# Performance work log

Measured on AMD Instinct MI355X. Metric: run time of the kernel, lower is better.

## Reference

```python
import jax, jax.numpy as jnp
import numpy as np
from math import sqrt

D_MODEL = 1024
N_HEADS = 16
E = D_MODEL // N_HEADS  # d_keys = d_values = 64


def setup_inputs() -> dict:
    key = jax.random.key(0)
    ks = jax.random.split(key, 11)
    B, L, S = 2, 2048, 2048
    s = 1.0 / sqrt(D_MODEL)
    return {
        "queries": jax.random.normal(ks[0], (B, L, D_MODEL), jnp.float32),
        "keys": jax.random.normal(ks[1], (B, S, D_MODEL), jnp.float32),
        "values": jax.random.normal(ks[2], (B, S, D_MODEL), jnp.float32),
        "Wq": jax.random.normal(ks[3], (D_MODEL, D_MODEL), jnp.float32) * s,
        "bq": jnp.zeros((D_MODEL,), jnp.float32),
        "Wk": jax.random.normal(ks[4], (D_MODEL, D_MODEL), jnp.float32) * s,
        "bk": jnp.zeros((D_MODEL,), jnp.float32),
        "Wv": jax.random.normal(ks[5], (D_MODEL, D_MODEL), jnp.float32) * s,
        "bv": jnp.zeros((D_MODEL,), jnp.float32),
        "Wo": jax.random.normal(ks[6], (D_MODEL, D_MODEL), jnp.float32) * s,
        "bo": jnp.zeros((D_MODEL,), jnp.float32),
    }


def reference(queries, keys, values, Wq, bq, Wk, bk, Wv, bv, Wo, bo):
    B, L, _ = queries.shape
    S = keys.shape[1]
    H = N_HEADS
    # projections -> [B, L/S, H, E]
    q = (queries @ Wq + bq).reshape(B, L, H, E)
    k = (keys @ Wk + bk).reshape(B, S, H, E)
    v = (values @ Wv + bv).reshape(B, S, H, E)
    scale = 1.0 / sqrt(E)
    scores = jnp.einsum('blhe,bshe->bhls', q, k)  # [B,H,L,S]
    A = jax.nn.softmax(scale * scores, axis=-1)   # dropout = identity (eval)
    V = jnp.einsum('bhls,bshd->blhd', A, v)       # [B,L,H,E]
    out = V.reshape(B, L, H * E) @ Wo + bo
    return out
```

## Files before the change

kernel.cpp:

```cpp
#include <hip/hip_runtime.h>
#include <hip/hip_bf16.h>
#include <stdint.h>

#define BATCH 2
#define SEQ   2048
#define DM    1024
#define NH    16
#define EH    64
#define MROWS (BATCH*SEQ)

typedef __attribute__((ext_vector_type(8))) short  short8;
typedef __attribute__((ext_vector_type(4))) float  floatx4;
typedef __attribute__((ext_vector_type(8))) unsigned short ushort8v;
typedef __attribute__((ext_vector_type(4))) unsigned short ushort4v;

__device__ __forceinline__ unsigned short f2bf(float f) {
    return (unsigned short)((__float_as_uint(f) + 0x8000u) >> 16);
}

__device__ __forceinline__ void gload_lds16(const void* g, void* l) {
    __builtin_amdgcn_global_load_lds(
        (const __attribute__((address_space(1))) unsigned int*)g,
        (__attribute__((address_space(3))) unsigned int*)l, 16, 0, 0);
}

__global__ __launch_bounds__(256)
void transpose_w(const float* __restrict__ W0, const float* __restrict__ W1,
                 const float* __restrict__ W2, const float* __restrict__ W3,
                 unsigned short* __restrict__ T0, unsigned short* __restrict__ T1,
                 unsigned short* __restrict__ T2, unsigned short* __restrict__ T3,
                 int zbase)
{
    int z = zbase + blockIdx.z;
    const float* W = (z == 0) ? W0 : (z == 1) ? W1 : (z == 2) ? W2 : W3;
    unsigned short* T = (z == 0) ? T0 : (z == 1) ? T1 : (z == 2) ? T2 : T3;
    __shared__ float t[32][33];
    const int tid = threadIdx.x;
    const int k0 = blockIdx.y * 32, n0 = blockIdx.x * 32;
    {
        int r = tid >> 3, c4 = (tid & 7) * 4;
        float4 u = *(const float4*)&W[(size_t)(k0 + r) * DM + n0 + c4];
        t[r][c4 + 0] = u.x; t[r][c4 + 1] = u.y; t[r][c4 + 2] = u.z; t[r][c4 + 3] = u.w;
    }
    __syncthreads();
    {
        int n = tid >> 3, k4 = (tid & 7) * 4;
        ushort4v o;
        o[0] = f2bf(t[k4 + 0][n]); o[1] = f2bf(t[k4 + 1][n]);
        o[2] = f2bf(t[k4 + 2][n]); o[3] = f2bf(t[k4 + 3][n]);
        *(ushort4v*)&T[(size_t)(n0 + n) * DM + k0 + k4] = o;
    }
}

struct ProjArgs {
    const float* act[3];
    const unsigned short* wt[3];
    const float* bias[3];
    unsigned short* C[3];
    float oscale[3];
};

__global__ __launch_bounds__(256)
void proj_qkv(ProjArgs pa)
{
    const int z = blockIdx.z;
    const bool vt = (z == 2);
    const int linear = (int)(blockIdx.x + gridDim.x * blockIdx.y);
    int rb, cb;
    if (!vt) { rb = linear & 31; cb = linear >> 5; }
    else     { cb = linear & 31; rb = linear >> 5; }
    const int row0 = rb * 128, col0 = cb * 128;

    const float* act = pa.act[z];
    const unsigned short* wt = pa.wt[z];

    __shared__ unsigned short As[128 * 32];
    __shared__ unsigned short Bs[128 * 32];

    const int tid = threadIdx.x;
    const int lane = tid & 63, w = tid >> 6;
    const int lane15 = lane & 15, quad = lane >> 4;

    floatx4 acc[2][8] = {};

    for (int kt = 0; kt < DM; kt += 32) {
        __syncthreads();
        if (!vt) {
#pragma unroll
            for (int rr = 0; rr < 2; ++rr) {
                int c = rr * 256 + tid;
                int row = c >> 2, kel = (c & 3) * 8;
                const float* p = &act[(size_t)(row0 + row) * DM + kt + kel];
                float4 u0 = *(const float4*)p;
                float4 u1 = *(const float4*)(p + 4);
                ushort8v o8;
                o8[0] = f2bf(u0.x); o8[1] = f2bf(u0.y); o8[2] = f2bf(u0.z); o8[3] = f2bf(u0.w);
                o8[4] = f2bf(u1.x); o8[5] = f2bf(u1.y); o8[6] = f2bf(u1.z); o8[7] = f2bf(u1.w);
                *(ushort8v*)&As[(size_t)c * 8] = o8;
            }
#pragma unroll
            for (int rr = 0; rr < 2; ++rr) {
                int c = rr * 256 + w * 64 + lane;
                int row = c >> 2, kel = (c & 3) * 8;
                gload_lds16(&wt[(size_t)(col0 + row) * DM + kt + kel],
                            (char*)Bs + (size_t)(rr * 256 + w * 64) * 16);
            }
        } else {
#pragma unroll
            for (int rr = 0; rr < 2; ++rr) {
                int c = rr * 256 + w * 64 + lane;
                int row = c >> 2, kel = (c & 3) * 8;
                gload_lds16(&wt[(size_t)(row0 + row) * DM + kt + kel],
                            (char*)As + (size_t)(rr * 256 + w * 64) * 16);
            }
#pragma unroll
            for (int rr = 0; rr < 2; ++rr) {
                int c = rr * 256 + tid;
                int row = c >> 2, kel = (c & 3) * 8;
                const float* p = &act[(size_t)(col0 + row) * DM + kt + kel];
                float4 u0 = *(const float4*)p;
                float4 u1 = *(const float4*)(p + 4);
                ushort8v o8;
                o8[0] = f2bf(u0.x); o8[1] = f2bf(u0.y); o8[2] = f2bf(u0.z); o8[3] = f2bf(u0.w);
                o8[4] = f2bf(u1.x); o8[5] = f2bf(u1.y); o8[6] = f2bf(u1.z); o8[7] = f2bf(u1.w);
                *(ushort8v*)&Bs[(size_t)c * 8] = o8;
            }
        }
        __syncthreads();

        short8 af[2], bf[8];
#pragma unroll
        for (int i = 0; i < 2; ++i)
            af[i] = *(const short8*)&As[(w * 32 + i * 16 + lane15) * 32 + quad * 8];
#pragma unroll
        for (int j = 0; j < 8; ++j)
            bf[j] = *(const short8*)&Bs[(j * 16 + lane15) * 32 + quad * 8];
#pragma unroll
        for (int i = 0; i < 2; ++i)
#pragma unroll
            for (int j = 0; j < 8; ++j)
                acc[i][j] = __builtin_amdgcn_mfma_f32_16x16x32_bf16(af[i], bf[j], acc[i][j], 0, 0, 0);
    }

    const float* bias = pa.bias[z];
    const float os = pa.oscale[z];
    unsigned short* C = pa.C[z];
#pragma unroll
    for (int i = 0; i < 2; ++i) {
#pragma unroll
        for (int j = 0; j < 8; ++j) {
#pragma unroll
            for (int r = 0; r < 4; ++r) {
                int row = row0 + w * 32 + i * 16 + quad * 4 + r;
                int col = col0 + j * 16 + lane15;
                if (!vt) {
                    float v = (acc[i][j][r] + bias[col]) * os;
                    int b = row >> 11, l = row & (SEQ - 1);
                    int h = col >> 6,  e = col & (EH - 1);
                    C[((size_t)(b * NH + h) * SEQ + l) * EH + e] = f2bf(v);
                } else {
                    float v = acc[i][j][r] + bias[row];
                    int h = row >> 6,  e = row & (EH - 1);
                    int b = col >> 11, l = col & (SEQ - 1);
                    C[((size_t)(b * NH + h) * EH + e) * SEQ + l] = f2bf(v);
                }
            }
        }
    }
}

__global__ __launch_bounds__(256)
void gemm_out(const unsigned short* __restrict__ ctx,
              const unsigned short* __restrict__ WoT,
              const float* __restrict__ bo,
              float* __restrict__ out)
{
    const int linear = (int)(blockIdx.x + gridDim.x * blockIdx.y);
    const int rb = linear & 31, cb = linear >> 5;
    const int row0 = rb * 128, col0 = cb * 64;

    __shared__ unsigned short As[128 * 32];
    __shared__ unsigned short Bs[64 * 32];

    const int tid = threadIdx.x;
    const int lane = tid & 63, w = tid >> 6;
    const int lane15 = lane & 15, quad = lane >> 4;

    floatx4 acc[2][4] = {};

    for (int kt = 0; kt < DM; kt += 32) {
        __syncthreads();
#pragma unroll
        for (int rr = 0; rr < 2; ++rr) {
            int c = rr * 256 + w * 64 + lane;
            int row = c >> 2, kel = (c & 3) * 8;
            gload_lds16(&ctx[(size_t)(row0 + row) * DM + kt + kel],
                        (char*)As + (size_t)(rr * 256 + w * 64) * 16);
        }
        {
            int c = w * 64 + lane;
            int row = c >> 2, kel = (c & 3) * 8;
            gload_lds16(&WoT[(size_t)(col0 + row) * DM + kt + kel],
                        (char*)Bs + (size_t)(w * 64) * 16);
        }
        __syncthreads();

        short8 af[2], bf[4];
#pragma unroll
        for (int i = 0; i < 2; ++i)
            af[i] = *(const short8*)&As[(w * 32 + i * 16 + lane15) * 32 + quad * 8];
#pragma unroll
        for (int j = 0; j < 4; ++j)
            bf[j] = *(const short8*)&Bs[(j * 16 + lane15) * 32 + quad * 8];
#pragma unroll
        for (int i = 0; i < 2; ++i)
#pragma unroll
            for (int j = 0; j < 4; ++j)
                acc[i][j] = __builtin_amdgcn_mfma_f32_16x16x32_bf16(af[i], bf[j], acc[i][j], 0, 0, 0);
    }

#pragma unroll
    for (int i = 0; i < 2; ++i)
#pragma unroll
        for (int j = 0; j < 4; ++j)
#pragma unroll
            for (int r = 0; r < 4; ++r) {
                int row = row0 + w * 32 + i * 16 + quad * 4 + r;
                int col = col0 + j * 16 + lane15;
                out[(size_t)row * DM + col] = acc[i][j][r] + bo[col];
            }
}

__device__ __forceinline__ void stage_kv(const unsigned short* __restrict__ Kp,
                                         const unsigned short* __restrict__ Vp,
                                         int st, unsigned short* ksb, unsigned short* vsb,
                                         int w, int lane)
{
#pragma unroll
    for (int rr = 0; rr < 2; ++rr) {
        int p = rr * 256 + w * 64 + lane;
        int row = p >> 3;
        int gch = (p & 7) ^ (row & 7);
        gload_lds16(&Kp[(size_t)(st + row) * EH + gch * 8],
                    ksb + (size_t)(rr * 256 + w * 64) * 8);
        gload_lds16(&Vp[(size_t)row * SEQ + st + gch * 8],
                    vsb + (size_t)(rr * 256 + w * 64) * 8);
    }
}

__global__ __launch_bounds__(256)
void attn_mfma(const unsigned short* __restrict__ Qh,
               const unsigned short* __restrict__ Kh,
               const unsigned short* __restrict__ Vt,
               unsigned short* __restrict__ ctx)
{
    __shared__ unsigned short Ks[2][64 * 64];
    __shared__ unsigned short Vs[2][64 * 64];
    __shared__ unsigned short Ps[128][72];

    const int tid = threadIdx.x;
    const int lane = tid & 63, w = tid >> 6;
    const int lane15 = lane & 15, quad = lane >> 4;
    const int qt = blockIdx.x, h = blockIdx.y, b = blockIdx.z;
    const size_t bh = (size_t)(b * NH + h);
    const unsigned short* Kp = Kh + bh * SEQ * EH;
    const unsigned short* Vp = Vt + bh * EH * SEQ;

    short8 qf[2][2];
    {
        const unsigned short* Qp =
            Qh + (bh * SEQ + (size_t)qt * 128 + w * 32 + lane15) * EH;
#pragma unroll
        for (int ks = 0; ks < 2; ++ks) {
            qf[0][ks] = *(const short8*)(Qp + ks * 32 + quad * 8);
            qf[1][ks] = *(const short8*)(Qp + 16 * EH + ks * 32 + quad * 8);
        }
    }
    short8 ones;
#pragma unroll
    for (int i = 0; i < 8; ++i) ones[i] = (short)0x3F80;

    floatx4 o[2][4] = {};
    floatx4 lacc[2] = {};

    stage_kv(Kp, Vp, 0, Ks[0], Vs[0], w, lane);
    __syncthreads();
    int cur = 0;

    for (int st = 0; st < SEQ; st += 64) {
        int nxt = cur ^ 1;
        if (st + 64 < SEQ)
            stage_kv(Kp, Vp, st + 64, Ks[nxt], Vs[nxt], w, lane);
        const unsigned short* ksb = Ks[cur];
        const unsigned short* vsb = Vs[cur];

        floatx4 sacc[4][2] = {};
#pragma unroll
        for (int ts = 0; ts < 4; ++ts) {
#pragma unroll
            for (int ks = 0; ks < 2; ++ks) {
                short8 kf = *(const short8*)&ksb[((ts * 16 + lane15) << 6) +
                                                 ((((ks << 2) + quad) ^ (lane15 & 7)) << 3)];
                sacc[ts][0] = __builtin_amdgcn_mfma_f32_16x16x32_bf16(kf, qf[0][ks], sacc[ts][0], 0, 0, 0);
                sacc[ts][1] = __builtin_amdgcn_mfma_f32_16x16x32_bf16(kf, qf[1][ks], sacc[ts][1], 0, 0, 0);
            }
        }

#pragma unroll
        for (int ts = 0; ts < 4; ++ts)
#pragma unroll
            for (int nq = 0; nq < 2; ++nq) {
                unsigned int u0 = __float_as_uint(__builtin_amdgcn_exp2f(sacc[ts][nq][0])) + 0x8000u;
                unsigned int u1 = __float_as_uint(__builtin_amdgcn_exp2f(sacc[ts][nq][1])) + 0x8000u;
                unsigned int u2 = __float_as_uint(__builtin_amdgcn_exp2f(sacc[ts][nq][2])) + 0x8000u;
                unsigned int u3 = __float_as_uint(__builtin_amdgcn_exp2f(sacc[ts][nq][3])) + 0x8000u;
                uint2 pk;
                pk.x = (u0 >> 16) | (u1 & 0xFFFF0000u);
                pk.y = (u2 >> 16) | (u3 & 0xFFFF0000u);
                *(uint2*)&Ps[w * 32 + nq * 16 + lane15][ts * 16 + quad * 4] = pk;
            }

#pragma unroll
        for (int ks = 0; ks < 2; ++ks) {
            short8 pf[2];
#pragma unroll
            for (int mt = 0; mt < 2; ++mt) {
                pf[mt] = *(const short8*)&Ps[w * 32 + mt * 16 + lane15][ks * 32 + quad * 8];
                lacc[mt] = __builtin_amdgcn_mfma_f32_16x16x32_bf16(pf[mt], ones, lacc[mt], 0, 0, 0);
            }
#pragma unroll
            for (int t2 = 0; t2 < 4; ++t2) {
                short8 vf = *(const short8*)&vsb[((t2 * 16 + lane15) << 6) +
                                                 ((((ks << 2) + quad) ^ (lane15 & 7)) << 3)];
                o[0][t2] = __builtin_amdgcn_mfma_f32_16x16x32_bf16(pf[0], vf, o[0][t2], 0, 0, 0);
                o[1][t2] = __builtin_amdgcn_mfma_f32_16x16x32_bf16(pf[1], vf, o[1][t2], 0, 0, 0);
            }
        }
        __syncthreads();
        cur = nxt;
    }

#pragma unroll
    for (int mt = 0; mt < 2; ++mt) {
        float inv[4];
#pragma unroll
        for (int r = 0; r < 4; ++r) inv[r] = 1.0f / lacc[mt][r];
#pragma unroll
        for (int t2 = 0; t2 < 4; ++t2)
#pragma unroll
            for (int r = 0; r < 4; ++r) {
                int q = qt * 128 + w * 32 + mt * 16 + quad * 4 + r;
                int col = h * EH + t2 * 16 + lane15;
                ctx[((size_t)(b * SEQ + q)) * DM + col] = f2bf(o[mt][t2][r] * inv[r]);
            }
    }
}

extern "C" void kernel_launch(void* const* d_in, const int* in_sizes, int n_in,
                              void* d_out, int out_size, void* d_ws, size_t ws_size,
                              hipStream_t stream)
{
    const float* queries = (const float*)d_in[0];
    const float* keys    = (const float*)d_in[1];
    const float* values  = (const float*)d_in[2];
    const float* Wq = (const float*)d_in[3];
    const float* bq = (const float*)d_in[4];
    const float* Wk = (const float*)d_in[5];
    const float* bk = (const float*)d_in[6];
    const float* Wv = (const float*)d_in[7];
    const float* bv = (const float*)d_in[8];
    const float* Wo = (const float*)d_in[9];
    const float* bo = (const float*)d_in[10];
    float* out = (float*)d_out;

    unsigned short* ws = (unsigned short*)d_ws;
    const size_t MAT = (size_t)MROWS * DM;
    const size_t WSZ = (size_t)DM * DM;
    unsigned short* Qhp = ws;
    unsigned short* Khp = ws + MAT;
    unsigned short* Vtp = ws + 2 * MAT;
    unsigned short* ctx = ws + 3 * MAT;
    unsigned short* WqT = ctx;
    unsigned short* WkT = ctx + WSZ;
    unsigned short* WvT = ctx + 2 * WSZ;
    unsigned short* WoT = ws;

    const float qscale = 0.125f * 1.44269504088896f;

    transpose_w<<<dim3(DM / 32, DM / 32, 3), 256, 0, stream>>>(
        Wq, Wk, Wv, Wo, WqT, WkT, WvT, WoT, 0);

    ProjArgs pa;
    pa.act[0] = queries; pa.act[1] = keys; pa.act[2] = values;
    pa.wt[0] = WqT;      pa.wt[1] = WkT;   pa.wt[2] = WvT;
    pa.bias[0] = bq;     pa.bias[1] = bk;  pa.bias[2] = bv;
    pa.C[0] = Qhp;       pa.C[1] = Khp;    pa.C[2] = Vtp;
    pa.oscale[0] = qscale; pa.oscale[1] = 1.f; pa.oscale[2] = 1.f;
    proj_qkv<<<dim3(8, 32, 3), 256, 0, stream>>>(pa);

    attn_mfma<<<dim3(SEQ / 128, NH, BATCH), 256, 0, stream>>>(Qhp, Khp, Vtp, ctx);

    transpose_w<<<dim3(DM / 32, DM / 32, 1), 256, 0, stream>>>(
        Wq, Wk, Wv, Wo, WqT, WkT, WvT, WoT, 3);

    gemm_out<<<dim3(16, 32), 256, 0, stream>>>(ctx, WoT, bo, out);
}
```

Baseline: 245.5 us.

## Prefetch fp32 activations into registers in QKV projection; remap attention block order

The QKV projection now loads the next k-tile's fp32 activations into registers right after the barrier, so their global latency overlaps the MFMA work of the current tile. The separate V-transposed branch is merged into one code path that selects destination buffers by pointer. The attention kernel remaps block indices so that consecutive blocks cover different batch-head pairs for the same query tile. The intent is to change cache and L2 locality across concurrently running blocks. The prefetch adds register pressure, which may lower occupancy.

```diff
diff --git a/kernel.cpp b/kernel.cpp
--- a/kernel.cpp
+++ b/kernel.cpp
@@ -73,9 +73,13 @@
 
     const float* act = pa.act[z];
     const unsigned short* wt = pa.wt[z];
+    const int actBase = vt ? col0 : row0;
+    const int wtBase  = vt ? row0 : col0;
 
     __shared__ unsigned short As[128 * 32];
     __shared__ unsigned short Bs[128 * 32];
+    unsigned short* convDst  = vt ? Bs : As;
+    unsigned short* asyncDst = vt ? As : Bs;
 
     const int tid = threadIdx.x;
     const int lane = tid & 63, w = tid >> 6;
@@ -83,50 +87,41 @@
 
     floatx4 acc[2][8] = {};
 
+    float4 pre[4];
+    {
+        const float* p0 = &act[(size_t)(actBase + (tid >> 2)) * DM + ((tid & 3) * 8)];
+        const float* p1 = &act[(size_t)(actBase + ((256 + tid) >> 2)) * DM + ((tid & 3) * 8)];
+        pre[0] = *(const float4*)p0; pre[1] = *(const float4*)(p0 + 4);
+        pre[2] = *(const float4*)p1; pre[3] = *(const float4*)(p1 + 4);
+    }
+
     for (int kt = 0; kt < DM; kt += 32) {
         __syncthreads();
-        if (!vt) {
-#pragma unroll
-            for (int rr = 0; rr < 2; ++rr) {
-                int c = rr * 256 + tid;
-                int row = c >> 2, kel = (c & 3) * 8;
-                const float* p = &act[(size_t)(row0 + row) * DM + kt + kel];
-                float4 u0 = *(const float4*)p;
-                float4 u1 = *(const float4*)(p + 4);
-                ushort8v o8;
-                o8[0] = f2bf(u0.x); o8[1] = f2bf(u0.y); o8[2] = f2bf(u0.z); o8[3] = f2bf(u0.w);
-                o8[4] = f2bf(u1.x); o8[5] = f2bf(u1.y); o8[6] = f2bf(u1.z); o8[7] = f2bf(u1.w);
-                *(ushort8v*)&As[(size_t)c * 8] = o8;
-            }
-#pragma unroll
-            for (int rr = 0; rr < 2; ++rr) {
-                int c = rr * 256 + w * 64 + lane;
-                int row = c >> 2, kel = (c & 3) * 8;
-                gload_lds16(&wt[(size_t)(col0 + row) * DM + kt + kel],
-                            (char*)Bs + (size_t)(rr * 256 + w * 64) * 16);
-            }
-        } else {
-#pragma unroll
-            for (int rr = 0; rr < 2; ++rr) {
-                int c = rr * 256 + w * 64 + lane;
-                int row = c >> 2, kel = (c & 3) * 8;
-                gload_lds16(&wt[(size_t)(row0 + row) * DM + kt + kel],
-                            (char*)As + (size_t)(rr * 256 + w * 64) * 16);
-            }
-#pragma unroll
-            for (int rr = 0; rr < 2; ++rr) {
-                int c = rr * 256 + tid;
-                int row = c >> 2, kel = (c & 3) * 8;
-                const float* p = &act[(size_t)(col0 + row) * DM + kt + kel];
-                float4 u0 = *(const float4*)p;
-                float4 u1 = *(const float4*)(p + 4);
-                ushort8v o8;
-                o8[0] = f2bf(u0.x); o8[1] = f2bf(u0.y); o8[2] = f2bf(u0.z); o8[3] = f2bf(u0.w);
-                o8[4] = f2bf(u1.x); o8[5] = f2bf(u1.y); o8[6] = f2bf(u1.z); o8[7] = f2bf(u1.w);
-                *(ushort8v*)&Bs[(size_t)c * 8] = o8;
-            }
+#pragma unroll
+        for (int rr = 0; rr < 2; ++rr) {
+            int c = rr * 256 + tid;
+            ushort8v o8;
+            float4 u0 = pre[rr * 2], u1 = pre[rr * 2 + 1];
+            o8[0] = f2bf(u0.x); o8[1] = f2bf(u0.y); o8[2] = f2bf(u0.z); o8[3] = f2bf(u0.w);
+            o8[4] = f2bf(u1.x); o8[5] = f2bf(u1.y); o8[6] = f2bf(u1.z); o8[7] = f2bf(u1.w);
+            *(ushort8v*)&convDst[(size_t)c * 8] = o8;
+        }
+#pragma unroll
+        for (int rr = 0; rr < 2; ++rr) {
+            int c = rr * 256 + w * 64 + lane;
+            int row = c >> 2, kel = (c & 3) * 8;
+            gload_lds16(&wt[(size_t)(wtBase + row) * DM + kt + kel],
+                        (char*)asyncDst + (size_t)(rr * 256 + w * 64) * 16);
         }
         __syncthreads();
+
+        if (kt + 32 < DM) {
+            int kn = kt + 32;
+            const float* p0 = &act[(size_t)(actBase + (tid >> 2)) * DM + kn + ((tid & 3) * 8)];
+            const float* p1 = &act[(size_t)(actBase + ((256 + tid) >> 2)) * DM + kn + ((tid & 3) * 8)];
+            pre[0] = *(const float4*)p0; pre[1] = *(const float4*)(p0 + 4);
+            pre[2] = *(const float4*)p1; pre[3] = *(const float4*)(p1 + 4);
+        }
 
         short8 af[2], bf[8];
 #pragma unroll
@@ -261,7 +256,12 @@
     const int tid = threadIdx.x;
     const int lane = tid & 63, w = tid >> 6;
     const int lane15 = lane & 15, quad = lane >> 4;
-    const int qt = blockIdx.x, h = blockIdx.y, b = blockIdx.z;
+
+    const int linear = (int)(blockIdx.x + 16 * (blockIdx.y + 16 * blockIdx.z));
+    const int bhid = linear & 31;
+    const int qt = linear >> 5;
+    const int h = bhid & 15, b = bhid >> 4;
+
     const size_t bh = (size_t)(b * NH + h);
     const unsigned short* Kp = Kh + bh * SEQ * EH;
     const unsigned short* Vp = Vt + bh * EH * SEQ;
```

Measured after the change: 233.5 us. -4.9%, faster.
